# Kernel tuning notes

Measured on AMD Instinct MI355X. Metric: run time of the kernel, lower is better.

## Reference

```python
import jax, jax.numpy as jnp
import numpy as np

N_NODES = 50000
N_EDGES = 800000
HEADS = 4
OUT_CH = 64
NEG_SLOPE = 0.2  # PyG GATConv default


def gat_conv(x, edge_index, W, att_src, att_dst, bias):
    """PyG GATConv (concat=True, add_self_loops=True, eval mode).
    x: [N, F_in], edge_index: [2, E] (row 0 = src, row 1 = dst).
    W: [F_in, H*C], att_src/att_dst: [1, H, C], bias: [H*C].
    """
    n = x.shape[0]
    loops = jnp.arange(n, dtype=edge_index.dtype)
    src = jnp.concatenate([edge_index[0], loops])  # [E+N]
    dst = jnp.concatenate([edge_index[1], loops])

    h = (x @ W).reshape(n, HEADS, OUT_CH)           # [N, H, C]
    a_src = jnp.sum(h * att_src, axis=-1)           # [N, H]
    a_dst = jnp.sum(h * att_dst, axis=-1)           # [N, H]

    e = a_src[src] + a_dst[dst]                     # [E+N, H]
    e = jax.nn.leaky_relu(e, NEG_SLOPE)

    # segment softmax over incoming edges of each dst node
    e_max = jax.ops.segment_max(e, dst, num_segments=n)   # [N, H]
    e_exp = jnp.exp(e - e_max[dst])
    denom = jax.ops.segment_sum(e_exp, dst, num_segments=n)
    alpha = e_exp / (denom[dst] + 1e-16)            # [E+N, H]

    msg = h[src] * alpha[:, :, None]                # [E+N, H, C]
    out = jax.ops.segment_sum(msg, dst, num_segments=n)   # [N, H, C]
    return out.reshape(n, HEADS * OUT_CH) + bias


def setup_inputs() -> dict:
    key = jax.random.key(0)
    ks = jax.random.split(key, 10)
    d_in = 256
    d_hid = HEADS * OUT_CH  # 256
    s_in = 1.0 / np.sqrt(d_in)
    s_hid = 1.0 / np.sqrt(d_hid)
    return {
        "x": jax.random.normal(ks[0], (N_NODES, d_in), dtype=jnp.float32),
        "edge_index": jax.random.randint(ks[1], (2, N_EDGES), 0, N_NODES, dtype=jnp.int32),
        "W1": jax.random.normal(ks[2], (d_in, d_hid), dtype=jnp.float32) * s_in,
        "att_src1": jax.random.normal(ks[3], (1, HEADS, OUT_CH), dtype=jnp.float32) * s_hid,
        "att_dst1": jax.random.normal(ks[4], (1, HEADS, OUT_CH), dtype=jnp.float32) * s_hid,
        "b1": jnp.zeros((d_hid,), dtype=jnp.float32),
        "W2": jax.random.normal(ks[5], (d_hid, d_hid), dtype=jnp.float32) * s_hid,
        "att_src2": jax.random.normal(ks[6], (1, HEADS, OUT_CH), dtype=jnp.float32) * s_hid,
        "att_dst2": jax.random.normal(ks[7], (1, HEADS, OUT_CH), dtype=jnp.float32) * s_hid,
        "b2": jnp.zeros((d_hid,), dtype=jnp.float32),
    }


def reference(x, edge_index, W1, att_src1, att_dst1, b1, W2, att_src2, att_dst2, b2):
    # layer 1 + ELU (dropout is identity in eval mode)
    h = gat_conv(x, edge_index, W1, att_src1, att_dst1, b1)
    h = jax.nn.elu(h)
    # layer 2 + ELU
    h = gat_conv(h, edge_index, W2, att_src2, att_dst2, b2)
    h = jax.nn.elu(h)
    return h
```

## Files before the change

### kernel.cpp

```cpp
#include <hip/hip_runtime.h>
#include <hip/hip_bf16.h>

#define N_NODES 50000
#define N_EDGES 800000

typedef __attribute__((ext_vector_type(8))) short short8;
typedef __attribute__((ext_vector_type(4))) float floatx4;
typedef __attribute__((ext_vector_type(2))) uint uintx2;

__device__ __forceinline__ ushort f2bf(float f) {
    uint u = __float_as_uint(f);
    uint r = u + 0x7FFFu + ((u >> 16) & 1u);
    return (ushort)(r >> 16);
}
__device__ __forceinline__ float bfu2f(ushort h) {
    return __uint_as_float(((uint)h) << 16);
}
__device__ __forceinline__ float bflo(uint u) { return __uint_as_float(u << 16); }
__device__ __forceinline__ float bfhi(uint u) { return __uint_as_float(u & 0xffff0000u); }
__device__ __forceinline__ float lrelu(float e) { return e >= 0.f ? e : 0.2f * e; }

__global__ void deg_kernel(const int* __restrict__ dst, int* __restrict__ cnt, int E) {
    int i = blockIdx.x * blockDim.x + threadIdx.x;
    if (i < E) atomicAdd(&cnt[dst[i]], 1);
}

__global__ __launch_bounds__(256) void scan1_kernel(const int* __restrict__ cnt,
                                                    int* __restrict__ excl,
                                                    int* __restrict__ partial, int n) {
    __shared__ int sd[256];
    int tid = threadIdx.x;
    int i = blockIdx.x * 256 + tid;
    int v = (i < n) ? cnt[i] : 0;
    sd[tid] = v;
    __syncthreads();
    #pragma unroll
    for (int off = 1; off < 256; off <<= 1) {
        int t = (tid >= off) ? sd[tid - off] : 0;
        __syncthreads();
        sd[tid] += t;
        __syncthreads();
    }
    if (i < n) excl[i] = sd[tid] - v;
    if (tid == 255) partial[blockIdx.x] = sd[255];
}

__global__ __launch_bounds__(256) void scan2_kernel(int* __restrict__ partial, int nb) {
    __shared__ int sd[256];
    int tid = threadIdx.x;
    int v = (tid < nb) ? partial[tid] : 0;
    sd[tid] = v;
    __syncthreads();
    #pragma unroll
    for (int off = 1; off < 256; off <<= 1) {
        int t = (tid >= off) ? sd[tid - off] : 0;
        __syncthreads();
        sd[tid] += t;
        __syncthreads();
    }
    if (tid < nb) partial[tid] = sd[tid] - v;
}

__global__ __launch_bounds__(256) void scan3_kernel(const int* __restrict__ excl,
                                                    const int* __restrict__ partial,
                                                    int* __restrict__ row_ptr,
                                                    int* __restrict__ row_tmp, int n) {
    int i = blockIdx.x * 256 + threadIdx.x;
    if (i < n) {
        int v = excl[i] + partial[blockIdx.x];
        row_ptr[i] = v;
        row_tmp[i] = v;
    }
    if (i == 0) row_ptr[n] = N_EDGES;
}

__global__ void scatter_kernel(const int* __restrict__ src, const int* __restrict__ dst,
                               int* __restrict__ row_tmp, int* __restrict__ sorted_src,
                               int* __restrict__ sorted_dst, int E) {
    int i = blockIdx.x * blockDim.x + threadIdx.x;
    if (i < E) {
        int d = dst[i];
        int p = atomicAdd(&row_tmp[d], 1);
        sorted_src[p] = src[i];
        sorted_dst[p] = d;
    }
}

__global__ void prep_w(const float* __restrict__ W1, const float* __restrict__ W2,
                       ushort* __restrict__ Wt1_hi, ushort* __restrict__ Wt1_lo,
                       ushort* __restrict__ Wt2_hi, ushort* __restrict__ Wt2_lo) {
    int n = threadIdx.x, k = blockIdx.x & 255;
    const float* W = (blockIdx.x < 256) ? W1 : W2;
    ushort* Wh = (blockIdx.x < 256) ? Wt1_hi : Wt2_hi;
    ushort* Wl = (blockIdx.x < 256) ? Wt1_lo : Wt2_lo;
    float v = W[k * 256 + n];
    ushort hb = f2bf(v);
    Wh[n * 256 + k] = hb;
    Wl[n * 256 + k] = f2bf(v - bfu2f(hb));
}

__global__ __launch_bounds__(256) void gemm_att_kernel(const float* __restrict__ A,
                                                       const ushort* __restrict__ Wt_hi,
                                                       const ushort* __restrict__ Wt_lo,
                                                       const float* __restrict__ att_s,
                                                       const float* __restrict__ att_d,
                                                       ushort* __restrict__ H,
                                                       float* __restrict__ a_src,
                                                       float* __restrict__ a_dst, int M) {
    const int ROWP = 40;
    __shared__ ushort hi_s[128 * ROWP];
    __shared__ ushort lo_s[128 * ROWP];
    const int tid = threadIdx.x;
    const int wave = tid >> 6, lane = tid & 63;
    const int quad = lane >> 4, l16 = lane & 15;
    const int brow = blockIdx.x * 64;
    const int coff = blockIdx.y * 128;
    const int mrow = brow + wave * 16 + l16;
    const int mload = (mrow < M) ? mrow : (M - 1);

    floatx4 acc[8];
    #pragma unroll
    for (int t = 0; t < 8; t++) acc[t] = (floatx4){0.f, 0.f, 0.f, 0.f};

    for (int k0 = 0; k0 < 256; k0 += 32) {
        __syncthreads();
        {
            int t = tid & 127;
            const ushort* g = ((tid < 128) ? Wt_hi : Wt_lo) + (size_t)(coff + t) * 256 + k0;
            ushort* d = ((tid < 128) ? hi_s : lo_s) + t * ROWP;
            #pragma unroll
            for (int i = 0; i < 4; i++)
                *reinterpret_cast<short8*>(d + i * 8) =
                    *reinterpret_cast<const short8*>(g + i * 8);
        }
        __syncthreads();
        const float* ap = A + (size_t)mload * 256 + k0 + quad * 8;
        float4 a0 = *reinterpret_cast<const float4*>(ap);
        float4 a1 = *reinterpret_cast<const float4*>(ap + 4);
        float av[8] = {a0.x, a0.y, a0.z, a0.w, a1.x, a1.y, a1.z, a1.w};
        short8 a_hi, a_lo;
        #pragma unroll
        for (int j = 0; j < 8; j++) {
            ushort hb = f2bf(av[j]);
            a_hi[j] = (short)hb;
            a_lo[j] = (short)f2bf(av[j] - bfu2f(hb));
        }
        #pragma unroll
        for (int t = 0; t < 8; t++) {
            int roff = (t * 16 + l16) * ROWP + quad * 8;
            short8 b_hi = *reinterpret_cast<const short8*>(&hi_s[roff]);
            short8 b_lo = *reinterpret_cast<const short8*>(&lo_s[roff]);
            acc[t] = __builtin_amdgcn_mfma_f32_16x16x32_bf16(a_hi, b_hi, acc[t], 0, 0, 0);
            acc[t] = __builtin_amdgcn_mfma_f32_16x16x32_bf16(a_hi, b_lo, acc[t], 0, 0, 0);
            acc[t] = __builtin_amdgcn_mfma_f32_16x16x32_bf16(a_lo, b_hi, acc[t], 0, 0, 0);
        }
    }
    const int hb = blockIdx.y * 2;
    float ps[2][4] = {}, pd[2][4] = {};
    #pragma unroll
    for (int t = 0; t < 8; t++) {
        int hh = t >> 2;
        float as_v = att_s[coff + t * 16 + l16];
        float ad_v = att_d[coff + t * 16 + l16];
        #pragma unroll
        for (int r = 0; r < 4; r++) {
            ps[hh][r] += acc[t][r] * as_v;
            pd[hh][r] += acc[t][r] * ad_v;
        }
    }
    #pragma unroll
    for (int off = 1; off < 16; off <<= 1) {
        #pragma unroll
        for (int hh = 0; hh < 2; hh++)
            #pragma unroll
            for (int r = 0; r < 4; r++) {
                ps[hh][r] += __shfl_xor(ps[hh][r], off, 64);
                pd[hh][r] += __shfl_xor(pd[hh][r], off, 64);
            }
    }
    if (l16 == 0) {
        #pragma unroll
        for (int r = 0; r < 4; r++) {
            int m = brow + wave * 16 + quad * 4 + r;
            if (m < M) {
                #pragma unroll
                for (int hh = 0; hh < 2; hh++) {
                    a_src[m * 4 + hb + hh] = ps[hh][r];
                    a_dst[m * 4 + hb + hh] = pd[hh][r];
                }
            }
        }
    }
    #pragma unroll
    for (int t = 0; t < 8; t++) {
        int col = coff + t * 16 + l16;
        int c = col & 63, hh = col >> 6;
        #pragma unroll
        for (int r = 0; r < 4; r++) {
            int m = brow + wave * 16 + quad * 4 + r;
            if (m < M) H[(size_t)m * 256 + c * 4 + hh] = f2bf(acc[t][r]);
        }
    }
}

__global__ __launch_bounds__(256) void ew_kernel(const float* __restrict__ a_src,
                                                 const float* __restrict__ a_dst,
                                                 const int* __restrict__ sorted_src,
                                                 const int* __restrict__ sorted_dst,
                                                 float* __restrict__ ew, int E) {
    int j = blockIdx.x * 256 + threadIdx.x;
    if (j >= E) return;
    int s = sorted_src[j], d = sorted_dst[j];
    float4 as_ = *reinterpret_cast<const float4*>(a_src + (size_t)s * 4);
    float4 ad_ = *reinterpret_cast<const float4*>(a_dst + (size_t)d * 4);
    float4 w;
    w.x = __expf(lrelu(as_.x + ad_.x));
    w.y = __expf(lrelu(as_.y + ad_.y));
    w.z = __expf(lrelu(as_.z + ad_.z));
    w.w = __expf(lrelu(as_.w + ad_.w));
    *reinterpret_cast<float4*>(ew + (size_t)j * 4) = w;
}

#define AGG_ACC(W_, V_)                                                     \
    do {                                                                    \
        a0 += (W_).x * bflo((V_).x); a1 += (W_).y * bfhi((V_).x);           \
        a2 += (W_).z * bflo((V_).y); a3 += (W_).w * bfhi((V_).y);           \
        dp0 += (W_).x; dp1 += (W_).y; dp2 += (W_).z; dp3 += (W_).w;         \
    } while (0)

__global__ __launch_bounds__(256) void agg_kernel(const ushort* __restrict__ H,
                                                  const float* __restrict__ a_src,
                                                  const float* __restrict__ a_dst,
                                                  const int* __restrict__ row_ptr,
                                                  const int* __restrict__ sorted_src,
                                                  const float* __restrict__ ew,
                                                  const float* __restrict__ bias,
                                                  float* __restrict__ out, int N) {
    const int lane = threadIdx.x & 63;
    const int i = __builtin_amdgcn_readfirstlane(blockIdx.x * 4 + (threadIdx.x >> 6));
    if (i >= N) return;
    const float4 asv = *reinterpret_cast<const float4*>(a_src + (size_t)i * 4);
    const float4 adv = *reinterpret_cast<const float4*>(a_dst + (size_t)i * 4);
    const float ws0 = __expf(lrelu(asv.x + adv.x)), ws1 = __expf(lrelu(asv.y + adv.y));
    const float ws2 = __expf(lrelu(asv.z + adv.z)), ws3 = __expf(lrelu(asv.w + adv.w));
    const int start = row_ptr[i], end = row_ptr[i + 1];

    float a0 = 0.f, a1 = 0.f, a2 = 0.f, a3 = 0.f;
    float dp0 = 0.f, dp1 = 0.f, dp2 = 0.f, dp3 = 0.f;
    const ushort* __restrict__ Hl = H + lane * 4;

    for (int j0 = start; j0 < end; j0 += 8) {
        int s[8];
        #pragma unroll
        for (int k = 0; k < 8; k++) s[k] = sorted_src[j0 + k];
        floatx4 w[8];
        #pragma unroll
        for (int k = 0; k < 8; k++)
            w[k] = *reinterpret_cast<const floatx4*>(ew + (size_t)(j0 + k) * 4);
        uintx2 hv[8];
        #pragma unroll
        for (int k = 0; k < 8; k++)
            hv[k] = *reinterpret_cast<const uintx2*>(Hl + (size_t)s[k] * 256);
        if (j0 + 8 <= end) {
            #pragma unroll
            for (int k = 0; k < 8; k++) AGG_ACC(w[k], hv[k]);
        } else {
            #pragma unroll
            for (int k = 0; k < 8; k++)
                if (j0 + k < end) AGG_ACC(w[k], hv[k]);
        }
    }
    {
        uintx2 hv = *reinterpret_cast<const uintx2*>(Hl + (size_t)i * 256);
        a0 += ws0 * bflo(hv.x); a1 += ws1 * bfhi(hv.x);
        a2 += ws2 * bflo(hv.y); a3 += ws3 * bfhi(hv.y);
    }
    const float r0 = 1.f / (dp0 + ws0 + 1e-16f), r1 = 1.f / (dp1 + ws1 + 1e-16f);
    const float r2 = 1.f / (dp2 + ws2 + 1e-16f), r3 = 1.f / (dp3 + ws3 + 1e-16f);
    float* op = out + (size_t)i * 256 + lane;
    float v;
    v = a0 * r0 + bias[lane];        v = (v > 0.f) ? v : expm1f(v);
    __builtin_nontemporal_store(v, op);
    v = a1 * r1 + bias[64 + lane];   v = (v > 0.f) ? v : expm1f(v);
    __builtin_nontemporal_store(v, op + 64);
    v = a2 * r2 + bias[128 + lane];  v = (v > 0.f) ? v : expm1f(v);
    __builtin_nontemporal_store(v, op + 128);
    v = a3 * r3 + bias[192 + lane];  v = (v > 0.f) ? v : expm1f(v);
    __builtin_nontemporal_store(v, op + 192);
}

extern "C" void kernel_launch(void* const* d_in, const int* in_sizes, int n_in,
                              void* d_out, int out_size, void* d_ws, size_t ws_size,
                              hipStream_t stream) {
    const float* x      = (const float*)d_in[0];
    const int*   eidx   = (const int*)d_in[1];
    const float* W1     = (const float*)d_in[2];
    const float* att_s1 = (const float*)d_in[3];
    const float* att_d1 = (const float*)d_in[4];
    const float* b1     = (const float*)d_in[5];
    const float* W2     = (const float*)d_in[6];
    const float* att_s2 = (const float*)d_in[7];
    const float* att_d2 = (const float*)d_in[8];
    const float* b2     = (const float*)d_in[9];
    float* out = (float*)d_out;

    const int N = N_NODES, E = N_EDGES;
    char* ws = (char*)d_ws;
    size_t off = 0;
    auto alloc = [&](size_t bytes) -> void* {
        void* p = ws + off;
        off += (bytes + 255) & ~(size_t)255;
        return p;
    };
    ushort* h       = (ushort*)alloc((size_t)N * 256 * sizeof(ushort));
    float*  ew      = (float*) alloc((size_t)E * 4 * sizeof(float));
    float*  a_src   = (float*) alloc((size_t)N * 4 * sizeof(float));
    float*  a_dst   = (float*) alloc((size_t)N * 4 * sizeof(float));
    int*    cnt     = (int*)   alloc((size_t)N * sizeof(int));
    int*    row_ptr = (int*)   alloc((size_t)(N + 1) * sizeof(int));
    int*    row_tmp = (int*)   alloc((size_t)N * sizeof(int));
    int*    sorted  = (int*)   alloc((size_t)E * sizeof(int));
    int*    sortedd = (int*)   alloc((size_t)E * sizeof(int));
    int*    excl    = (int*)   alloc((size_t)N * sizeof(int));
    int*    partial = (int*)   alloc(256 * sizeof(int));
    ushort* Wt1_hi  = (ushort*)alloc(256 * 256 * sizeof(ushort));
    ushort* Wt1_lo  = (ushort*)alloc(256 * 256 * sizeof(ushort));
    ushort* Wt2_hi  = (ushort*)alloc(256 * 256 * sizeof(ushort));
    ushort* Wt2_lo  = (ushort*)alloc(256 * 256 * sizeof(ushort));
    float*  x2      = out;
    (void)ws_size; (void)in_sizes; (void)n_in; (void)out_size;

    const int* e_src = eidx;
    const int* e_dst = eidx + E;
    const int nsb = (N + 255) / 256;
    const int neb = (E + 255) / 256;

    prep_w<<<512, 256, 0, stream>>>(W1, W2, Wt1_hi, Wt1_lo, Wt2_hi, Wt2_lo);
    hipMemsetAsync(cnt, 0, N * sizeof(int), stream);
    deg_kernel<<<neb, 256, 0, stream>>>(e_dst, cnt, E);
    scan1_kernel<<<nsb, 256, 0, stream>>>(cnt, excl, partial, N);
    scan2_kernel<<<1, 256, 0, stream>>>(partial, nsb);
    scan3_kernel<<<nsb, 256, 0, stream>>>(excl, partial, row_ptr, row_tmp, N);
    scatter_kernel<<<neb, 256, 0, stream>>>(e_src, e_dst, row_tmp, sorted, sortedd, E);

    dim3 ggrid((N + 63) / 64, 2);
    int nblk = (N + 3) / 4;
    gemm_att_kernel<<<ggrid, 256, 0, stream>>>(x, Wt1_hi, Wt1_lo, att_s1, att_d1,
                                               h, a_src, a_dst, N);
    ew_kernel<<<neb, 256, 0, stream>>>(a_src, a_dst, sorted, sortedd, ew, E);
    agg_kernel<<<nblk, 256, 0, stream>>>(h, a_src, a_dst, row_ptr, sorted, ew, b1, x2, N);
    gemm_att_kernel<<<ggrid, 256, 0, stream>>>(x2, Wt2_hi, Wt2_lo, att_s2, att_d2,
                                               h, a_src, a_dst, N);
    ew_kernel<<<neb, 256, 0, stream>>>(a_src, a_dst, sorted, sortedd, ew, E);
    agg_kernel<<<nblk, 256, 0, stream>>>(h, a_src, a_dst, row_ptr, sorted, ew, b2, out, N);
}
```

Before: 461.0 us.

## Compute all 256 GEMM columns per block with register-prefetched, swizzled weight tiles

The GEMM+attention kernel now has each block cover all 256 output columns (all four heads) instead of splitting columns across two blocks. The A tile is loaded and split into bf16 hi/lo once instead of twice, and the a_src/a_dst dot products are finished in one block. The next k-slice of weights and activations is prefetched into registers while MFMAs run on the current one, and the LDS layout is XOR-swizzled to avoid bank conflicts. The H output is written as packed 8-byte stores covering four heads at once. In exchange the block uses twice the LDS and accumulator registers, which may lower occupancy.

```diff
diff --git a/kernel.cpp b/kernel.cpp
--- a/kernel.cpp
+++ b/kernel.cpp
@@ -108,36 +108,59 @@
                                                        float* __restrict__ a_src,
                                                        float* __restrict__ a_dst, int M) {
     const int ROWP = 40;
-    __shared__ ushort hi_s[128 * ROWP];
-    __shared__ ushort lo_s[128 * ROWP];
+    __shared__ ushort hi_s[256 * ROWP];
+    __shared__ ushort lo_s[256 * ROWP];
     const int tid = threadIdx.x;
     const int wave = tid >> 6, lane = tid & 63;
     const int quad = lane >> 4, l16 = lane & 15;
     const int brow = blockIdx.x * 64;
-    const int coff = blockIdx.y * 128;
     const int mrow = brow + wave * 16 + l16;
     const int mload = (mrow < M) ? mrow : (M - 1);
 
-    floatx4 acc[8];
-    #pragma unroll
-    for (int t = 0; t < 8; t++) acc[t] = (floatx4){0.f, 0.f, 0.f, 0.f};
-
-    for (int k0 = 0; k0 < 256; k0 += 32) {
+    floatx4 acc[16];
+    #pragma unroll
+    for (int t = 0; t < 16; t++) acc[t] = (floatx4){0.f, 0.f, 0.f, 0.f};
+
+    short8 wh[4], wl[4];
+    const ushort* gh0 = Wt_hi + (size_t)tid * 256;
+    const ushort* gl0 = Wt_lo + (size_t)tid * 256;
+    const float* ap0 = A + (size_t)mload * 256 + quad * 8;
+    const int wsw = (tid >> 3) & 3;
+
+    #pragma unroll
+    for (int i = 0; i < 4; i++) {
+        wh[i] = *reinterpret_cast<const short8*>(gh0 + i * 8);
+        wl[i] = *reinterpret_cast<const short8*>(gl0 + i * 8);
+    }
+    float4 a0c = *reinterpret_cast<const float4*>(ap0);
+    float4 a1c = *reinterpret_cast<const float4*>(ap0 + 4);
+    float4 a0n, a1n;
+
+    for (int t = 0; t < 8; t++) {
         __syncthreads();
         {
-            int t = tid & 127;
-            const ushort* g = ((tid < 128) ? Wt_hi : Wt_lo) + (size_t)(coff + t) * 256 + k0;
-            ushort* d = ((tid < 128) ? hi_s : lo_s) + t * ROWP;
-            #pragma unroll
-            for (int i = 0; i < 4; i++)
-                *reinterpret_cast<short8*>(d + i * 8) =
-                    *reinterpret_cast<const short8*>(g + i * 8);
-        }
-        __syncthreads();
-        const float* ap = A + (size_t)mload * 256 + k0 + quad * 8;
-        float4 a0 = *reinterpret_cast<const float4*>(ap);
-        float4 a1 = *reinterpret_cast<const float4*>(ap + 4);
-        float av[8] = {a0.x, a0.y, a0.z, a0.w, a1.x, a1.y, a1.z, a1.w};
+            ushort* dh = hi_s + tid * ROWP;
+            ushort* dl = lo_s + tid * ROWP;
+            #pragma unroll
+            for (int i = 0; i < 4; i++) {
+                *reinterpret_cast<short8*>(dh + (i ^ wsw) * 8) = wh[i];
+                *reinterpret_cast<short8*>(dl + (i ^ wsw) * 8) = wl[i];
+            }
+        }
+        __syncthreads();
+        if (t < 7) {
+            const ushort* gh = gh0 + (t + 1) * 32;
+            const ushort* gl = gl0 + (t + 1) * 32;
+            #pragma unroll
+            for (int i = 0; i < 4; i++) {
+                wh[i] = *reinterpret_cast<const short8*>(gh + i * 8);
+                wl[i] = *reinterpret_cast<const short8*>(gl + i * 8);
+            }
+            const float* apn = ap0 + (t + 1) * 32;
+            a0n = *reinterpret_cast<const float4*>(apn);
+            a1n = *reinterpret_cast<const float4*>(apn + 4);
+        }
+        float av[8] = {a0c.x, a0c.y, a0c.z, a0c.w, a1c.x, a1c.y, a1c.z, a1c.w};
         short8 a_hi, a_lo;
         #pragma unroll
         for (int j = 0; j < 8; j++) {
@@ -146,22 +169,23 @@
             a_lo[j] = (short)f2bf(av[j] - bfu2f(hb));
         }
         #pragma unroll
-        for (int t = 0; t < 8; t++) {
-            int roff = (t * 16 + l16) * ROWP + quad * 8;
+        for (int tt = 0; tt < 16; tt++) {
+            int col = tt * 16 + l16;
+            int roff = col * ROWP + (quad ^ ((col >> 3) & 3)) * 8;
             short8 b_hi = *reinterpret_cast<const short8*>(&hi_s[roff]);
             short8 b_lo = *reinterpret_cast<const short8*>(&lo_s[roff]);
-            acc[t] = __builtin_amdgcn_mfma_f32_16x16x32_bf16(a_hi, b_hi, acc[t], 0, 0, 0);
-            acc[t] = __builtin_amdgcn_mfma_f32_16x16x32_bf16(a_hi, b_lo, acc[t], 0, 0, 0);
-            acc[t] = __builtin_amdgcn_mfma_f32_16x16x32_bf16(a_lo, b_hi, acc[t], 0, 0, 0);
-        }
-    }
-    const int hb = blockIdx.y * 2;
-    float ps[2][4] = {}, pd[2][4] = {};
-    #pragma unroll
-    for (int t = 0; t < 8; t++) {
+            acc[tt] = __builtin_amdgcn_mfma_f32_16x16x32_bf16(a_hi, b_hi, acc[tt], 0, 0, 0);
+            acc[tt] = __builtin_amdgcn_mfma_f32_16x16x32_bf16(a_hi, b_lo, acc[tt], 0, 0, 0);
+            acc[tt] = __builtin_amdgcn_mfma_f32_16x16x32_bf16(a_lo, b_hi, acc[tt], 0, 0, 0);
+        }
+        a0c = a0n; a1c = a1n;
+    }
+    float ps[4][4] = {}, pd[4][4] = {};
+    #pragma unroll
+    for (int t = 0; t < 16; t++) {
         int hh = t >> 2;
-        float as_v = att_s[coff + t * 16 + l16];
-        float ad_v = att_d[coff + t * 16 + l16];
+        float as_v = att_s[t * 16 + l16];
+        float ad_v = att_d[t * 16 + l16];
         #pragma unroll
         for (int r = 0; r < 4; r++) {
             ps[hh][r] += acc[t][r] * as_v;
@@ -171,7 +195,7 @@
     #pragma unroll
     for (int off = 1; off < 16; off <<= 1) {
         #pragma unroll
-        for (int hh = 0; hh < 2; hh++)
+        for (int hh = 0; hh < 4; hh++)
             #pragma unroll
             for (int r = 0; r < 4; r++) {
                 ps[hh][r] += __shfl_xor(ps[hh][r], off, 64);
@@ -184,21 +208,24 @@
             int m = brow + wave * 16 + quad * 4 + r;
             if (m < M) {
                 #pragma unroll
-                for (int hh = 0; hh < 2; hh++) {
-                    a_src[m * 4 + hb + hh] = ps[hh][r];
-                    a_dst[m * 4 + hb + hh] = pd[hh][r];
+                for (int hh = 0; hh < 4; hh++) {
+                    a_src[m * 4 + hh] = ps[hh][r];
+                    a_dst[m * 4 + hh] = pd[hh][r];
                 }
             }
         }
     }
     #pragma unroll
-    for (int t = 0; t < 8; t++) {
-        int col = coff + t * 16 + l16;
-        int c = col & 63, hh = col >> 6;
+    for (int cc = 0; cc < 4; cc++) {
         #pragma unroll
         for (int r = 0; r < 4; r++) {
             int m = brow + wave * 16 + quad * 4 + r;
-            if (m < M) H[(size_t)m * 256 + c * 4 + hh] = f2bf(acc[t][r]);
+            if (m < M) {
+                uintx2 pk;
+                pk.x = (uint)f2bf(acc[cc][r])     | ((uint)f2bf(acc[cc + 4][r]) << 16);
+                pk.y = (uint)f2bf(acc[cc + 8][r]) | ((uint)f2bf(acc[cc + 12][r]) << 16);
+                *reinterpret_cast<uintx2*>(H + (size_t)m * 256 + (cc * 16 + l16) * 4) = pk;
+            }
         }
     }
 }
@@ -343,7 +370,7 @@
     scan3_kernel<<<nsb, 256, 0, stream>>>(excl, partial, row_ptr, row_tmp, N);
     scatter_kernel<<<neb, 256, 0, stream>>>(e_src, e_dst, row_tmp, sorted, sortedd, E);
 
-    dim3 ggrid((N + 63) / 64, 2);
+    int ggrid = (N + 63) / 64;
     int nblk = (N + 3) / 4;
     gemm_att_kernel<<<ggrid, 256, 0, stream>>>(x, Wt1_hi, Wt1_lo, att_s1, att_d1,
                                                h, a_src, a_dst, N);
```

New measurement: 463.9 us. No clear change (+0.6%).

## Fold attention vectors into extra weight columns and restructure GEMM without LDS

Applied to the files above, without the earlier changes.

Precomputes W·att_src and W·att_dst as 8 extra columns (padded to 16) of the transposed split-bf16 weight, so the attention logits come out of an extra MFMA tile instead of a shuffle reduction. The GEMM now covers all 256 output columns per block with a 1D grid. It loads B fragments straight from global memory with register double-buffering instead of staging them through shared memory, and writes H with packed 8-byte stores. This removes the duplicate A reads of the two-column-block grid and the LDS barriers, at the cost of more registers (launch bounds 256,2) and uncached global B loads per wave.

```diff
diff --git a/kernel.cpp b/kernel.cpp
--- a/kernel.cpp
+++ b/kernel.cpp
@@ -86,119 +86,153 @@
     }
 }
 
-__global__ void prep_w(const float* __restrict__ W1, const float* __restrict__ W2,
-                       ushort* __restrict__ Wt1_hi, ushort* __restrict__ Wt1_lo,
-                       ushort* __restrict__ Wt2_hi, ushort* __restrict__ Wt2_lo) {
-    int n = threadIdx.x, k = blockIdx.x & 255;
-    const float* W = (blockIdx.x < 256) ? W1 : W2;
-    ushort* Wh = (blockIdx.x < 256) ? Wt1_hi : Wt2_hi;
-    ushort* Wl = (blockIdx.x < 256) ? Wt1_lo : Wt2_lo;
-    float v = W[k * 256 + n];
-    ushort hb = f2bf(v);
-    Wh[n * 256 + k] = hb;
-    Wl[n * 256 + k] = f2bf(v - bfu2f(hb));
-}
-
-__global__ __launch_bounds__(256) void gemm_att_kernel(const float* __restrict__ A,
-                                                       const ushort* __restrict__ Wt_hi,
-                                                       const ushort* __restrict__ Wt_lo,
-                                                       const float* __restrict__ att_s,
-                                                       const float* __restrict__ att_d,
-                                                       ushort* __restrict__ H,
-                                                       float* __restrict__ a_src,
-                                                       float* __restrict__ a_dst, int M) {
-    const int ROWP = 40;
-    __shared__ ushort hi_s[128 * ROWP];
-    __shared__ ushort lo_s[128 * ROWP];
+__global__ __launch_bounds__(320) void prep_w(const float* __restrict__ W1,
+                                              const float* __restrict__ W2,
+                                              const float* __restrict__ as1,
+                                              const float* __restrict__ ad1,
+                                              const float* __restrict__ as2,
+                                              const float* __restrict__ ad2,
+                                              ushort* __restrict__ Wt1_hi,
+                                              ushort* __restrict__ Wt1_lo,
+                                              ushort* __restrict__ Wt2_hi,
+                                              ushort* __restrict__ Wt2_lo) {
+    int t = threadIdx.x, k = blockIdx.x & 255;
+    int l1 = (blockIdx.x < 256);
+    const float* W = l1 ? W1 : W2;
+    const float* as_ = l1 ? as1 : as2;
+    const float* ad_ = l1 ? ad1 : ad2;
+    ushort* Wh = l1 ? Wt1_hi : Wt2_hi;
+    ushort* Wl = l1 ? Wt1_lo : Wt2_lo;
+    if (t < 256) {
+        float v = W[k * 256 + t];
+        ushort hb = f2bf(v);
+        Wh[t * 256 + k] = hb;
+        Wl[t * 256 + k] = f2bf(v - bfu2f(hb));
+    } else if (t < 264) {
+        int j = t - 256;
+        int h = j & 3;
+        const float* vec = (j < 4) ? as_ : ad_;
+        float acc = 0.f;
+        for (int c = 0; c < 64; c++) acc += W[k * 256 + h * 64 + c] * vec[h * 64 + c];
+        ushort hb = f2bf(acc);
+        Wh[t * 256 + k] = hb;
+        Wl[t * 256 + k] = f2bf(acc - bfu2f(hb));
+    } else if (t < 272) {
+        Wh[t * 256 + k] = 0;
+        Wl[t * 256 + k] = 0;
+    }
+}
+
+__global__ __launch_bounds__(256, 2) void gemm_att_kernel(const float* __restrict__ A,
+                                                          const ushort* __restrict__ Wt_hi,
+                                                          const ushort* __restrict__ Wt_lo,
+                                                          ushort* __restrict__ H,
+                                                          float* __restrict__ a_src,
+                                                          float* __restrict__ a_dst, int M) {
     const int tid = threadIdx.x;
     const int wave = tid >> 6, lane = tid & 63;
     const int quad = lane >> 4, l16 = lane & 15;
     const int brow = blockIdx.x * 64;
-    const int coff = blockIdx.y * 128;
-    const int mrow = brow + wave * 16 + l16;
-    const int mload = (mrow < M) ? mrow : (M - 1);
-
-    floatx4 acc[8];
-    #pragma unroll
-    for (int t = 0; t < 8; t++) acc[t] = (floatx4){0.f, 0.f, 0.f, 0.f};
-
-    for (int k0 = 0; k0 < 256; k0 += 32) {
-        __syncthreads();
-        {
-            int t = tid & 127;
-            const ushort* g = ((tid < 128) ? Wt_hi : Wt_lo) + (size_t)(coff + t) * 256 + k0;
-            ushort* d = ((tid < 128) ? hi_s : lo_s) + t * ROWP;
-            #pragma unroll
-            for (int i = 0; i < 4; i++)
-                *reinterpret_cast<short8*>(d + i * 8) =
-                    *reinterpret_cast<const short8*>(g + i * 8);
-        }
-        __syncthreads();
-        const float* ap = A + (size_t)mload * 256 + k0 + quad * 8;
-        float4 a0 = *reinterpret_cast<const float4*>(ap);
-        float4 a1 = *reinterpret_cast<const float4*>(ap + 4);
-        float av[8] = {a0.x, a0.y, a0.z, a0.w, a1.x, a1.y, a1.z, a1.w};
-        short8 a_hi, a_lo;
-        #pragma unroll
-        for (int j = 0; j < 8; j++) {
-            ushort hb = f2bf(av[j]);
-            a_hi[j] = (short)hb;
-            a_lo[j] = (short)f2bf(av[j] - bfu2f(hb));
-        }
-        #pragma unroll
-        for (int t = 0; t < 8; t++) {
-            int roff = (t * 16 + l16) * ROWP + quad * 8;
-            short8 b_hi = *reinterpret_cast<const short8*>(&hi_s[roff]);
-            short8 b_lo = *reinterpret_cast<const short8*>(&lo_s[roff]);
-            acc[t] = __builtin_amdgcn_mfma_f32_16x16x32_bf16(a_hi, b_hi, acc[t], 0, 0, 0);
-            acc[t] = __builtin_amdgcn_mfma_f32_16x16x32_bf16(a_hi, b_lo, acc[t], 0, 0, 0);
-            acc[t] = __builtin_amdgcn_mfma_f32_16x16x32_bf16(a_lo, b_hi, acc[t], 0, 0, 0);
-        }
-    }
-    const int hb = blockIdx.y * 2;
-    float ps[2][4] = {}, pd[2][4] = {};
+
+    floatx4 acc[4][4];
+    floatx4 accA[4];
+    #pragma unroll
+    for (int rg = 0; rg < 4; rg++) {
+        accA[rg] = (floatx4){0.f, 0.f, 0.f, 0.f};
+        #pragma unroll
+        for (int i = 0; i < 4; i++) acc[rg][i] = (floatx4){0.f, 0.f, 0.f, 0.f};
+    }
+
+    int ar[4];
+    #pragma unroll
+    for (int rg = 0; rg < 4; rg++) {
+        int r = brow + rg * 16 + l16;
+        ar[rg] = (r < M) ? r : (M - 1);
+    }
+    const size_t bofs = (size_t)(wave * 16 + l16) * 256 + quad * 8;
+    const ushort* bh0 = Wt_hi + bofs;
+    const ushort* bl0 = Wt_lo + bofs;
+    const ushort* bha0 = Wt_hi + (size_t)(256 + l16) * 256 + quad * 8;
+    const ushort* bla0 = Wt_lo + (size_t)(256 + l16) * 256 + quad * 8;
+
+    short8 bh[4], bl[4], bhn[4], bln[4];
+    float4 af0[4], af1[4];
+
+    #pragma unroll
+    for (int i = 0; i < 4; i++) {
+        bh[i] = *reinterpret_cast<const short8*>(bh0 + i * 64 * 256);
+        bl[i] = *reinterpret_cast<const short8*>(bl0 + i * 64 * 256);
+    }
+    #pragma unroll
+    for (int rg = 0; rg < 4; rg++) {
+        const float* ap = A + (size_t)ar[rg] * 256 + quad * 8;
+        af0[rg] = *reinterpret_cast<const float4*>(ap);
+        af1[rg] = *reinterpret_cast<const float4*>(ap + 4);
+    }
+
     #pragma unroll
     for (int t = 0; t < 8; t++) {
-        int hh = t >> 2;
-        float as_v = att_s[coff + t * 16 + l16];
-        float ad_v = att_d[coff + t * 16 + l16];
+        const int k0 = t * 32;
+        if (t < 7) {
+            #pragma unroll
+            for (int i = 0; i < 4; i++) {
+                bhn[i] = *reinterpret_cast<const short8*>(bh0 + i * 64 * 256 + k0 + 32);
+                bln[i] = *reinterpret_cast<const short8*>(bl0 + i * 64 * 256 + k0 + 32);
+            }
+        }
+        short8 bha = *reinterpret_cast<const short8*>(bha0 + k0);
+        short8 bla = *reinterpret_cast<const short8*>(bla0 + k0);
+        short8 ah[4], al[4];
+        #pragma unroll
+        for (int rg = 0; rg < 4; rg++) {
+            float av[8] = {af0[rg].x, af0[rg].y, af0[rg].z, af0[rg].w,
+                           af1[rg].x, af1[rg].y, af1[rg].z, af1[rg].w};
+            #pragma unroll
+            for (int j = 0; j < 8; j++) {
+                ushort hb = f2bf(av[j]);
+                ah[rg][j] = (short)hb;
+                al[rg][j] = (short)f2bf(av[j] - bfu2f(hb));
+            }
+        }
+        if (t < 7) {
+            #pragma unroll
+            for (int rg = 0; rg < 4; rg++) {
+                const float* ap = A + (size_t)ar[rg] * 256 + quad * 8 + k0 + 32;
+                af0[rg] = *reinterpret_cast<const float4*>(ap);
+                af1[rg] = *reinterpret_cast<const float4*>(ap + 4);
+            }
+        }
+        #pragma unroll
+        for (int rg = 0; rg < 4; rg++) {
+            #pragma unroll
+            for (int i = 0; i < 4; i++) {
+                acc[rg][i] = __builtin_amdgcn_mfma_f32_16x16x32_bf16(ah[rg], bh[i], acc[rg][i], 0, 0, 0);
+                acc[rg][i] = __builtin_amdgcn_mfma_f32_16x16x32_bf16(ah[rg], bl[i], acc[rg][i], 0, 0, 0);
+                acc[rg][i] = __builtin_amdgcn_mfma_f32_16x16x32_bf16(al[rg], bh[i], acc[rg][i], 0, 0, 0);
+            }
+            accA[rg] = __builtin_amdgcn_mfma_f32_16x16x32_bf16(ah[rg], bha, accA[rg], 0, 0, 0);
+            accA[rg] = __builtin_amdgcn_mfma_f32_16x16x32_bf16(ah[rg], bla, accA[rg], 0, 0, 0);
+            accA[rg] = __builtin_amdgcn_mfma_f32_16x16x32_bf16(al[rg], bha, accA[rg], 0, 0, 0);
+        }
+        #pragma unroll
+        for (int i = 0; i < 4; i++) { bh[i] = bhn[i]; bl[i] = bln[i]; }
+    }
+    #pragma unroll
+    for (int rg = 0; rg < 4; rg++) {
         #pragma unroll
         for (int r = 0; r < 4; r++) {
-            ps[hh][r] += acc[t][r] * as_v;
-            pd[hh][r] += acc[t][r] * ad_v;
-        }
-    }
-    #pragma unroll
-    for (int off = 1; off < 16; off <<= 1) {
-        #pragma unroll
-        for (int hh = 0; hh < 2; hh++)
-            #pragma unroll
-            for (int r = 0; r < 4; r++) {
-                ps[hh][r] += __shfl_xor(ps[hh][r], off, 64);
-                pd[hh][r] += __shfl_xor(pd[hh][r], off, 64);
-            }
-    }
-    if (l16 == 0) {
-        #pragma unroll
-        for (int r = 0; r < 4; r++) {
-            int m = brow + wave * 16 + quad * 4 + r;
+            int m = brow + rg * 16 + quad * 4 + r;
             if (m < M) {
-                #pragma unroll
-                for (int hh = 0; hh < 2; hh++) {
-                    a_src[m * 4 + hb + hh] = ps[hh][r];
-                    a_dst[m * 4 + hb + hh] = pd[hh][r];
+                uintx2 pk;
+                pk.x = (uint)f2bf(acc[rg][0][r]) | ((uint)f2bf(acc[rg][1][r]) << 16);
+                pk.y = (uint)f2bf(acc[rg][2][r]) | ((uint)f2bf(acc[rg][3][r]) << 16);
+                *reinterpret_cast<uintx2*>(H + (size_t)m * 256 + (wave * 16 + l16) * 4) = pk;
+                if (wave == 0) {
+                    float v = accA[rg][r];
+                    if (l16 < 4) a_src[m * 4 + l16] = v;
+                    else if (l16 < 8) a_dst[m * 4 + (l16 - 4)] = v;
                 }
             }
-        }
-    }
-    #pragma unroll
-    for (int t = 0; t < 8; t++) {
-        int col = coff + t * 16 + l16;
-        int c = col & 63, hh = col >> 6;
-        #pragma unroll
-        for (int r = 0; r < 4; r++) {
-            int m = brow + wave * 16 + quad * 4 + r;
-            if (m < M) H[(size_t)m * 256 + c * 4 + hh] = f2bf(acc[t][r]);
         }
     }
 }
@@ -323,10 +357,10 @@
     int*    sortedd = (int*)   alloc((size_t)E * sizeof(int));
     int*    excl    = (int*)   alloc((size_t)N * sizeof(int));
     int*    partial = (int*)   alloc(256 * sizeof(int));
-    ushort* Wt1_hi  = (ushort*)alloc(256 * 256 * sizeof(ushort));
-    ushort* Wt1_lo  = (ushort*)alloc(256 * 256 * sizeof(ushort));
-    ushort* Wt2_hi  = (ushort*)alloc(256 * 256 * sizeof(ushort));
-    ushort* Wt2_lo  = (ushort*)alloc(256 * 256 * sizeof(ushort));
+    ushort* Wt1_hi  = (ushort*)alloc(272 * 256 * sizeof(ushort));
+    ushort* Wt1_lo  = (ushort*)alloc(272 * 256 * sizeof(ushort));
+    ushort* Wt2_hi  = (ushort*)alloc(272 * 256 * sizeof(ushort));
+    ushort* Wt2_lo  = (ushort*)alloc(272 * 256 * sizeof(ushort));
     float*  x2      = out;
     (void)ws_size; (void)in_sizes; (void)n_in; (void)out_size;
 
@@ -335,7 +369,8 @@
     const int nsb = (N + 255) / 256;
     const int neb = (E + 255) / 256;
 
-    prep_w<<<512, 256, 0, stream>>>(W1, W2, Wt1_hi, Wt1_lo, Wt2_hi, Wt2_lo);
+    prep_w<<<512, 320, 0, stream>>>(W1, W2, att_s1, att_d1, att_s2, att_d2,
+                                    Wt1_hi, Wt1_lo, Wt2_hi, Wt2_lo);
     hipMemsetAsync(cnt, 0, N * sizeof(int), stream);
     deg_kernel<<<neb, 256, 0, stream>>>(e_dst, cnt, E);
     scan1_kernel<<<nsb, 256, 0, stream>>>(cnt, excl, partial, N);
@@ -343,14 +378,12 @@
     scan3_kernel<<<nsb, 256, 0, stream>>>(excl, partial, row_ptr, row_tmp, N);
     scatter_kernel<<<neb, 256, 0, stream>>>(e_src, e_dst, row_tmp, sorted, sortedd, E);
 
-    dim3 ggrid((N + 63) / 64, 2);
+    int ggrid = (N + 63) / 64;
     int nblk = (N + 3) / 4;
-    gemm_att_kernel<<<ggrid, 256, 0, stream>>>(x, Wt1_hi, Wt1_lo, att_s1, att_d1,
-                                               h, a_src, a_dst, N);
+    gemm_att_kernel<<<ggrid, 256, 0, stream>>>(x, Wt1_hi, Wt1_lo, h, a_src, a_dst, N);
     ew_kernel<<<neb, 256, 0, stream>>>(a_src, a_dst, sorted, sortedd, ew, E);
     agg_kernel<<<nblk, 256, 0, stream>>>(h, a_src, a_dst, row_ptr, sorted, ew, b1, x2, N);
-    gemm_att_kernel<<<ggrid, 256, 0, stream>>>(x2, Wt2_hi, Wt2_lo, att_s2, att_d2,
-                                               h, a_src, a_dst, N);
+    gemm_att_kernel<<<ggrid, 256, 0, stream>>>(x2, Wt2_hi, Wt2_lo, h, a_src, a_dst, N);
     ew_kernel<<<neb, 256, 0, stream>>>(a_src, a_dst, sorted, sortedd, ew, E);
     agg_kernel<<<nblk, 256, 0, stream>>>(h, a_src, a_dst, row_ptr, sorted, ew, b2, out, N);
 }
```

After: 488.5 us. +6.0%, slower.
